# Kernel optimization log

Measured on AMD Instinct MI355X. Metric: run time of the kernel, lower is better.

The kernel has to match this reference:

```python
import jax, jax.numpy as jnp
import numpy as np

N_NODES, N_EDGES, B = 16384, 262144, 128
FEAT, HEADS, OUT_DIM, EMBED, PROT_LEN, VOCAB = 78, 10, 128, 128, 1000, 26
NEG_SLOPE = 0.2


def _gat_conv(x, src, dst, W, a_src, a_dst, b, heads, out_c):
    """PyG-style GATConv (concat heads), eval mode (no dropout)."""
    n = x.shape[0]
    xl = (x @ W).reshape(n, heads, out_c)                    # [N,H,C]
    alpha_s = jnp.einsum('nhc,hc->nh', xl, a_src)            # [N,H]
    alpha_d = jnp.einsum('nhc,hc->nh', xl, a_dst)
    e = jax.nn.leaky_relu(alpha_s[src] + alpha_d[dst], NEG_SLOPE)  # [E,H]
    # scatter-softmax over destination neighborhoods
    m = jax.ops.segment_max(e, dst, num_segments=n)
    m = jnp.where(jnp.isfinite(m), m, 0.0)
    p = jnp.exp(e - m[dst])
    s = jax.ops.segment_sum(p, dst, num_segments=n)
    alpha = p / (s[dst] + 1e-16)                             # [E,H]
    out = jax.ops.segment_sum(alpha[:, :, None] * xl[src], dst, num_segments=n)
    return out.reshape(n, heads * out_c) + b


def setup_inputs() -> dict:
    key = jax.random.key(0)
    ks = jax.random.split(key, 24)
    inp = {}
    inp['x'] = jax.random.normal(ks[0], (N_NODES, FEAT), jnp.float32)
    inp['edge_index'] = jax.random.randint(ks[1], (2, N_EDGES), 0, N_NODES)
    inp['batch'] = jnp.sort(jax.random.randint(ks[2], (N_NODES,), 0, B))
    inp['target'] = jax.random.randint(ks[3], (B, PROT_LEN), 0, VOCAB)
    s = 0.05
    rn = lambda k, sh: jax.random.normal(k, sh, jnp.float32) * s
    inp['W1'] = rn(ks[4], (FEAT, HEADS * FEAT))
    inp['att_src1'] = rn(ks[5], (HEADS, FEAT))
    inp['att_dst1'] = rn(ks[6], (HEADS, FEAT))
    inp['b1'] = jnp.zeros((HEADS * FEAT,), jnp.float32)
    # GAT layer 2: 780 -> 128, 1 head
    inp['W2'] = rn(ks[7], (HEADS * FEAT, OUT_DIM))
    inp['att_src2'] = rn(ks[8], (1, OUT_DIM))
    inp['att_dst2'] = rn(ks[9], (1, OUT_DIM))
    inp['b2'] = jnp.zeros((OUT_DIM,), jnp.float32)
    inp['fc_g1_w'] = rn(ks[10], (OUT_DIM, OUT_DIM)); inp['fc_g1_b'] = jnp.zeros((OUT_DIM,), jnp.float32)
    inp['emb'] = rn(ks[11], (VOCAB, EMBED))
    inp['conv_w'] = rn(ks[12], (32, PROT_LEN, 8)); inp['conv_b'] = jnp.zeros((32,), jnp.float32)
    inp['fc_xt_w'] = rn(ks[13], (32 * 121, OUT_DIM)); inp['fc_xt_b'] = jnp.zeros((OUT_DIM,), jnp.float32)
    inp['fc1_w'] = rn(ks[14], (256, 1024)); inp['fc1_b'] = jnp.zeros((1024,), jnp.float32)
    inp['fc2_w'] = rn(ks[15], (1024, 256)); inp['fc2_b'] = jnp.zeros((256,), jnp.float32)
    inp['out_w'] = rn(ks[16], (256, 1)); inp['out_b'] = jnp.zeros((1,), jnp.float32)
    return inp


def reference(x, edge_index, batch, target, W1, att_src1, att_dst1, b1,
              W2, att_src2, att_dst2, b2, fc_g1_w, fc_g1_b, emb, conv_w, conv_b,
              fc_xt_w, fc_xt_b, fc1_w, fc1_b, fc2_w, fc2_b, out_w, out_b):
    n = x.shape[0]
    # add self-loops (PyG GATConv default)
    loops = jnp.arange(n, dtype=edge_index.dtype)
    src = jnp.concatenate([edge_index[0], loops])
    dst = jnp.concatenate([edge_index[1], loops])
    # drug graph branch (eval: dropout = identity)
    h = jax.nn.elu(_gat_conv(x, src, dst, W1, att_src1, att_dst1, b1, HEADS, FEAT))
    h = _gat_conv(h, src, dst, W2, att_src2, att_dst2, b2, 1, OUT_DIM)
    h = jax.nn.relu(h)
    # global max pool per graph
    g = jax.ops.segment_max(h, batch, num_segments=B)
    g = jnp.where(jnp.isfinite(g), g, 0.0)
    g = jax.nn.relu(g @ fc_g1_w + fc_g1_b)                   # [B,128]
    # protein branch: embedding -> conv1d over embed axis (channels = seq pos)
    e = emb[target]                                          # [B,1000,128]
    c = jax.lax.conv_general_dilated(e, conv_w, (1,), 'VALID',
                                     dimension_numbers=('NCH', 'OIH', 'NCH'))
    c = jax.nn.relu(c + conv_b[None, :, None])               # [B,32,121]
    xt = c.reshape(-1, 32 * 121) @ fc_xt_w + fc_xt_b         # [B,128]
    # fused head
    xc = jnp.concatenate([g, xt], axis=1)                    # [B,256]
    xc = jax.nn.relu(xc @ fc1_w + fc1_b)
    xc = jax.nn.relu(xc @ fc2_w + fc2_b)
    return xc @ out_w + out_b                                # [B,1]
```

## Files before the change

kernel.cpp:

```cpp
#include <hip/hip_runtime.h>
#include <hip/hip_bf16.h>

using bf16 = __hip_bfloat16;

#define NN 16384
#define NE 262144
#define ET (NE + NN)
#define NB 128
#define FEAT 78
#define HEADS 10
#define D1 780
#define OD 128
#define PL 1000
#define VOC 26
#define SLOPE 0.2f

__global__ void k_hist(const int* __restrict__ ei, int* __restrict__ cnt){
    int e = blockIdx.x*256 + threadIdx.x;
    if (e >= ET) return;
    int dst = (e < NE) ? ei[NE + e] : (e - NE);
    atomicAdd(&cnt[dst], 1);
}

__global__ __launch_bounds__(1024) void k_scan(const int* __restrict__ cnt, int* __restrict__ off){
    __shared__ int ps[1024];
    int t = threadIdx.x;
    int loc[16]; int s = 0;
#pragma unroll
    for (int j = 0; j < 16; ++j){ loc[j] = cnt[t*16 + j]; s += loc[j]; }
    ps[t] = s; __syncthreads();
    for (int d = 1; d < 1024; d <<= 1){
        int v = (t >= d) ? ps[t - d] : 0;
        __syncthreads();
        ps[t] += v;
        __syncthreads();
    }
    int run = (t == 0) ? 0 : ps[t - 1];
#pragma unroll
    for (int j = 0; j < 16; ++j){ off[t*16 + j] = run; run += loc[j]; }
    if (t == 1023) off[NN] = run;
}

__global__ void k_fill(const int* __restrict__ ei, const int* __restrict__ off,
                       int* __restrict__ cur, int* __restrict__ csrc){
    int e = blockIdx.x*256 + threadIdx.x;
    if (e >= ET) return;
    int src, dst;
    if (e < NE){ src = ei[e]; dst = ei[NE + e]; } else { src = e - NE; dst = src; }
    int p = off[dst] + atomicAdd(&cur[dst], 1);
    csrc[p] = src;
}

__global__ __launch_bounds__(256) void k_alpha1x(const float* __restrict__ x, const float* __restrict__ W1,
                                                 const float* __restrict__ asw, const float* __restrict__ adw,
                                                 float* __restrict__ as1, float* __restrict__ ad1){
    __shared__ float xs[64*79];
    __shared__ float va[D1], vd[D1];
    int n0 = blockIdx.x * 64, t = threadIdx.x;
    for (int i = t; i < 64*FEAT; i += 256){
        int n = i / FEAT, k = i % FEAT;
        xs[n*79 + k] = x[(size_t)n0*FEAT + i];
    }
    for (int idx = t; idx < D1; idx += 256){
        int h = idx / FEAT, k = idx % FEAT;
        const float* wr = W1 + (size_t)k*D1 + h*FEAT;
        const float* pa = asw + h*FEAT;
        const float* pd = adw + h*FEAT;
        float a = 0.f, d = 0.f;
        for (int j = 0; j < FEAT; ++j){ float w = wr[j]; a += w*pa[j]; d += w*pd[j]; }
        va[idx] = a; vd[idx] = d;
    }
    __syncthreads();
    for (int p = t; p < 64*HEADS; p += 256){
        int h = p >> 6, nl = p & 63;
        const float* xr = xs + nl*79;
        const float* pa = va + h*FEAT; const float* pd = vd + h*FEAT;
        float a = 0.f, d = 0.f;
        for (int k = 0; k < FEAT; ++k){ float xv = xr[k]; a += xv*pa[k]; d += xv*pd[k]; }
        as1[(size_t)(n0 + nl)*HEADS + h] = a;
        ad1[(size_t)(n0 + nl)*HEADS + h] = d;
    }
}

__global__ __launch_bounds__(64) void k_gat1x(const float* __restrict__ x, const float* __restrict__ as1,
                                              const float* __restrict__ ad1, const int* __restrict__ off,
                                              const int* __restrict__ csrc,
                                              float* __restrict__ agg){
    int dst = blockIdx.x, lane = threadIdx.x;
    int beg = off[dst], end = off[dst + 1];
    int deg = end - beg;
    float adh[HEADS];
#pragma unroll
    for (int h = 0; h < HEADS; ++h) adh[h] = ad1[(size_t)dst*HEADS + h];
    int s0 = 0;
    float p[HEADS], mx[HEADS];
#pragma unroll
    for (int h = 0; h < HEADS; ++h){ mx[h] = -1e30f; p[h] = 0.f; }
    if (lane < deg){
        s0 = csrc[beg + lane];
#pragma unroll
        for (int h = 0; h < HEADS; ++h){
            float v = as1[(size_t)s0*HEADS + h] + adh[h];
            v = v > 0.f ? v : SLOPE*v;
            p[h] = v; mx[h] = v;
        }
    }
    if (deg > 64){
        for (int e = beg + 64 + lane; e < end; e += 64){
            int s = csrc[e];
#pragma unroll
            for (int h = 0; h < HEADS; ++h){
                float v = as1[(size_t)s*HEADS + h] + adh[h];
                v = v > 0.f ? v : SLOPE*v;
                mx[h] = fmaxf(mx[h], v);
            }
        }
    }
#pragma unroll
    for (int h = 0; h < HEADS; ++h)
        for (int o = 32; o; o >>= 1) mx[h] = fmaxf(mx[h], __shfl_xor(mx[h], o));
    float sm[HEADS];
#pragma unroll
    for (int h = 0; h < HEADS; ++h) sm[h] = 0.f;
    if (lane < deg){
#pragma unroll
        for (int h = 0; h < HEADS; ++h){ p[h] = __expf(p[h] - mx[h]); sm[h] = p[h]; }
    }
    if (deg > 64){
        for (int e = beg + 64 + lane; e < end; e += 64){
            int s = csrc[e];
#pragma unroll
            for (int h = 0; h < HEADS; ++h){
                float v = as1[(size_t)s*HEADS + h] + adh[h];
                v = v > 0.f ? v : SLOPE*v;
                sm[h] += __expf(v - mx[h]);
            }
        }
    }
    float inv[HEADS];
#pragma unroll
    for (int h = 0; h < HEADS; ++h){
        for (int o = 32; o; o >>= 1) sm[h] += __shfl_xor(sm[h], o);
        inv[h] = 1.f/(sm[h] + 1e-16f);
        p[h] = (lane < deg) ? p[h]*inv[h] : 0.f;
    }
    float acc1[HEADS], acc2[HEADS];
#pragma unroll
    for (int h = 0; h < HEADS; ++h){ acc1[h] = 0.f; acc2[h] = 0.f; }
    int cnt0 = deg < 64 ? deg : 64;
    for (int c0 = 0; c0 < cnt0; c0 += 16){
        float r1[16], r2[16];
#pragma unroll
        for (int i = 0; i < 16; ++i){
            int s = __shfl(s0, c0 + i);
            const float* xr = x + (size_t)s*FEAT;
            r1[i] = xr[lane];
            r2[i] = (lane < FEAT - 64) ? xr[64 + lane] : 0.f;
        }
#pragma unroll
        for (int i = 0; i < 16; ++i){
            if (c0 + i < cnt0){
#pragma unroll
                for (int h = 0; h < HEADS; ++h){
                    float al = __shfl(p[h], c0 + i);
                    acc1[h] += al*r1[i];
                    acc2[h] += al*r2[i];
                }
            }
        }
    }
    if (deg > 64){
        for (int base = beg + 64; base < end; base += 64){
            int cnt = min(64, end - base);
            int s1 = 0;
            float pp[HEADS];
#pragma unroll
            for (int h = 0; h < HEADS; ++h) pp[h] = 0.f;
            if (lane < cnt){
                s1 = csrc[base + lane];
#pragma unroll
                for (int h = 0; h < HEADS; ++h){
                    float v = as1[(size_t)s1*HEADS + h] + adh[h];
                    v = v > 0.f ? v : SLOPE*v;
                    pp[h] = __expf(v - mx[h])*inv[h];
                }
            }
            for (int c0 = 0; c0 < cnt; c0 += 16){
                float r1[16], r2[16];
#pragma unroll
                for (int i = 0; i < 16; ++i){
                    int s = __shfl(s1, c0 + i);
                    const float* xr = x + (size_t)s*FEAT;
                    r1[i] = xr[lane];
                    r2[i] = (lane < FEAT - 64) ? xr[64 + lane] : 0.f;
                }
#pragma unroll
                for (int i = 0; i < 16; ++i){
                    if (c0 + i < cnt){
#pragma unroll
                        for (int h = 0; h < HEADS; ++h){
                            float al = __shfl(pp[h], c0 + i);
                            acc1[h] += al*r1[i];
                            acc2[h] += al*r2[i];
                        }
                    }
                }
            }
        }
    }
#pragma unroll
    for (int h = 0; h < HEADS; ++h)
        agg[(size_t)dst*D1 + h*FEAT + lane] = acc1[h];
    if (lane < FEAT - 64){
#pragma unroll
        for (int h = 0; h < HEADS; ++h)
            agg[(size_t)dst*D1 + h*FEAT + 64 + lane] = acc2[h];
    }
}

__global__ __launch_bounds__(256) void k_post1(const float* __restrict__ agg, const float* __restrict__ W1,
                                               const float* __restrict__ b1, float* __restrict__ h1){
    __shared__ float w1s[FEAT][80];
    __shared__ float ags[64][81];
    __shared__ float bsh[FEAT];
    int ht = blockIdx.x >> 8;
    int nt = blockIdx.x & 255;
    int n0 = nt * 64;
    int t = threadIdx.x;
    for (int i = t; i < FEAT*FEAT; i += 256){
        int k = i / FEAT, j = i % FEAT;
        w1s[k][j] = W1[(size_t)k*D1 + ht*FEAT + j];
    }
    for (int i = t; i < 64*FEAT; i += 256){
        int r = i / FEAT, k = i % FEAT;
        ags[r][k] = agg[(size_t)(n0 + r)*D1 + ht*FEAT + k];
    }
    if (t < FEAT) bsh[t] = b1[ht*FEAT + t];
    __syncthreads();
    if (t < 208){
        int rg = t / 13, cg = t % 13;
        int c0 = cg*6;
        float acc[4][6];
#pragma unroll
        for (int i = 0; i < 4; ++i)
#pragma unroll
            for (int j = 0; j < 6; ++j) acc[i][j] = 0.f;
        for (int k = 0; k < FEAT; ++k){
            float av[4];
#pragma unroll
            for (int i = 0; i < 4; ++i) av[i] = ags[rg*4 + i][k];
            float2 w01 = *(const float2*)&w1s[k][c0];
            float2 w23 = *(const float2*)&w1s[k][c0 + 2];
            float2 w45 = *(const float2*)&w1s[k][c0 + 4];
            float wv[6] = {w01.x, w01.y, w23.x, w23.y, w45.x, w45.y};
#pragma unroll
            for (int i = 0; i < 4; ++i)
#pragma unroll
                for (int j = 0; j < 6; ++j) acc[i][j] += av[i]*wv[j];
        }
#pragma unroll
        for (int i = 0; i < 4; ++i){
#pragma unroll
            for (int j = 0; j < 6; ++j){
                float v = acc[i][j] + bsh[c0 + j];
                v = v > 0.f ? v : __expf(v) - 1.f;
                h1[(size_t)(n0 + rg*4 + i)*D1 + ht*FEAT + c0 + j] = v;
            }
        }
    }
}

#define KC 39
#define KS 4
#define KSEG 195
__global__ __launch_bounds__(256) void k_gemm2(const float* __restrict__ h1, const float* __restrict__ W2,
                                               float* __restrict__ xlp){
    __shared__ __align__(16) float as[KC][68];
    __shared__ __align__(16) float ws[KC][128];
    int bid = blockIdx.x;
    int ks = bid & (KS - 1);
    int r0 = (bid >> 2) * 64;
    int t = threadIdx.x;
    int rg = t >> 5, jq = t & 31;
    float acc[8][4];
#pragma unroll
    for (int i = 0; i < 8; ++i)
#pragma unroll
        for (int j = 0; j < 4; ++j) acc[i][j] = 0.f;
    for (int kc = ks*KSEG; kc < ks*KSEG + KSEG; kc += KC){
        for (int i = t; i < 64*KC; i += 256){
            int r = i / KC, k = i % KC;
            as[k][r] = h1[(size_t)(r0 + r)*D1 + kc + k];
        }
        for (int i = t; i < KC*128; i += 256){
            int k = i >> 7, j = i & 127;
            ws[k][j] = W2[(size_t)(kc + k)*OD + j];
        }
        __syncthreads();
        for (int k = 0; k < KC; ++k){
            float4 a0 = *(const float4*)&as[k][rg*8];
            float4 a1 = *(const float4*)&as[k][rg*8 + 4];
            float4 w4 = *(const float4*)&ws[k][jq*4];
            float av[8] = {a0.x, a0.y, a0.z, a0.w, a1.x, a1.y, a1.z, a1.w};
            float wv[4] = {w4.x, w4.y, w4.z, w4.w};
#pragma unroll
            for (int i = 0; i < 8; ++i)
#pragma unroll
                for (int j = 0; j < 4; ++j) acc[i][j] += av[i]*wv[j];
        }
        __syncthreads();
    }
    float* dst = xlp + (size_t)ks*NN*OD;
#pragma unroll
    for (int i = 0; i < 8; ++i){
        float4 o4 = make_float4(acc[i][0], acc[i][1], acc[i][2], acc[i][3]);
        *(float4*)&dst[(size_t)(r0 + rg*8 + i)*OD + jq*4] = o4;
    }
}

__global__ __launch_bounds__(128) void k_red(const float* __restrict__ xlp,
                                             const float* __restrict__ s2w, const float* __restrict__ d2w,
                                             float* __restrict__ xl2,
                                             float* __restrict__ as2, float* __restrict__ ad2){
    const size_t Q = (size_t)NN*OD/4;
    int t = threadIdx.x;
    size_t fi = (size_t)blockIdx.x*128 + t;
    const float4* P = (const float4*)xlp;
    float4 a = P[fi], b = P[fi + Q], c = P[fi + 2*Q], d = P[fi + 3*Q];
    float4 v = make_float4(a.x+b.x+c.x+d.x, a.y+b.y+c.y+d.y,
                           a.z+b.z+c.z+d.z, a.w+b.w+c.w+d.w);
    ((float4*)xl2)[fi] = v;
    int cc = (t & 31)*4;
    float sa = v.x*s2w[cc] + v.y*s2w[cc+1] + v.z*s2w[cc+2] + v.w*s2w[cc+3];
    float sd = v.x*d2w[cc] + v.y*d2w[cc+1] + v.z*d2w[cc+2] + v.w*d2w[cc+3];
#pragma unroll
    for (int o = 16; o; o >>= 1){ sa += __shfl_xor(sa, o); sd += __shfl_xor(sd, o); }
    if ((t & 31) == 0){
        int n = blockIdx.x*4 + (t >> 5);
        as2[n] = sa; ad2[n] = sd;
    }
}

__global__ __launch_bounds__(64) void k_gat2(const float* __restrict__ xl2, const float* __restrict__ as2,
                                             const float* __restrict__ ad2, const int* __restrict__ off,
                                             const int* __restrict__ csrc, const float* __restrict__ b2,
                                             float* __restrict__ h2){
    int dst = blockIdx.x, lane = threadIdx.x;
    int beg = off[dst], end = off[dst + 1];
    int deg = end - beg;
    float ad = ad2[dst];
    int s0 = 0; float v0 = -1e30f;
    if (lane < deg){
        s0 = csrc[beg + lane];
        float v = as2[s0] + ad;
        v0 = v > 0.f ? v : SLOPE*v;
    }
    float m = v0;
    if (deg > 64){
        for (int e = beg + 64 + lane; e < end; e += 64){
            float v = as2[csrc[e]] + ad; v = v > 0.f ? v : SLOPE*v;
            m = fmaxf(m, v);
        }
    }
    for (int o = 32; o; o >>= 1) m = fmaxf(m, __shfl_xor(m, o));
    float pe = (lane < deg) ? __expf(v0 - m) : 0.f;
    float sm = pe;
    if (deg > 64){
        for (int e = beg + 64 + lane; e < end; e += 64){
            float v = as2[csrc[e]] + ad; v = v > 0.f ? v : SLOPE*v;
            sm += __expf(v - m);
        }
    }
    for (int o = 32; o; o >>= 1) sm += __shfl_xor(sm, o);
    float inv = 1.f / (sm + 1e-16f);
    float p = pe * inv;
    float a0 = 0.f, a1 = 0.f;
    int cnt0 = deg < 64 ? deg : 64;
    for (int c0 = 0; c0 < cnt0; c0 += 16){
        float r1[16], r2[16];
#pragma unroll
        for (int i = 0; i < 16; ++i){
            int s = __shfl(s0, c0 + i);
            r1[i] = xl2[(size_t)s*OD + lane];
            r2[i] = xl2[(size_t)s*OD + 64 + lane];
        }
#pragma unroll
        for (int i = 0; i < 16; ++i){
            if (c0 + i < cnt0){
                float al = __shfl(p, c0 + i);
                a0 += al*r1[i];
                a1 += al*r2[i];
            }
        }
    }
    if (deg > 64){
        for (int base = beg + 64; base < end; base += 64){
            int cnt = min(64, end - base);
            int s1 = 0; float pp = 0.f;
            if (lane < cnt){
                s1 = csrc[base + lane];
                float v = as2[s1] + ad; v = v > 0.f ? v : SLOPE*v;
                pp = __expf(v - m) * inv;
            }
            for (int c0 = 0; c0 < cnt; c0 += 16){
                float r1[16], r2[16];
#pragma unroll
                for (int i = 0; i < 16; ++i){
                    int s = __shfl(s1, c0 + i);
                    r1[i] = xl2[(size_t)s*OD + lane];
                    r2[i] = xl2[(size_t)s*OD + 64 + lane];
                }
#pragma unroll
                for (int i = 0; i < 16; ++i){
                    if (c0 + i < cnt){
                        float al = __shfl(pp, c0 + i);
                        a0 += al*r1[i];
                        a1 += al*r2[i];
                    }
                }
            }
        }
    }
    float o0 = a0 + b2[lane];      o0 = o0 > 0.f ? o0 : 0.f;
    float o1 = a1 + b2[64 + lane]; o1 = o1 > 0.f ? o1 : 0.f;
    h2[(size_t)dst*OD + lane] = o0;
    h2[(size_t)dst*OD + 64 + lane] = o1;
}

__global__ __launch_bounds__(128) void k_poolfc(const float* __restrict__ h2, const int* __restrict__ batch,
                                                const float* __restrict__ w, const float* __restrict__ bias,
                                                float* __restrict__ gfc){
    __shared__ float row[OD];
    int b = blockIdx.x, t = threadIdx.x;
    int lo = 0, hi = NN;
    while (lo < hi){ int mid = (lo + hi) >> 1; if (batch[mid] < b) lo = mid + 1; else hi = mid; }
    int s0 = lo;
    lo = s0; hi = NN;
    while (lo < hi){ int mid = (lo + hi) >> 1; if (batch[mid] < b + 1) lo = mid + 1; else hi = mid; }
    int s1 = lo;
    float mx = 0.f;
    for (int n = s0; n < s1; ++n) mx = fmaxf(mx, h2[(size_t)n*OD + t]);
    row[t] = mx;
    __syncthreads();
    float acc = 0.f;
    for (int k = 0; k < OD; ++k) acc += row[k] * w[k*OD + t];
    acc += bias[t];
    gfc[b*OD + t] = acc > 0.f ? acc : 0.f;
}

__global__ __launch_bounds__(256) void k_wt(const float* __restrict__ convw, float* __restrict__ wt){
    int idx = blockIdx.x*256 + threadIdx.x;
    int i = idx >> 8, ok = idx & 255;
    wt[idx] = convw[(size_t)(ok >> 3)*PL*8 + (size_t)i*8 + (ok & 7)];
}

__global__ __launch_bounds__(256) void k_abuild(const int* __restrict__ target, const float* __restrict__ wt,
                                                float* __restrict__ Ag){
    __shared__ int Ai[VOC][256];
    __shared__ int tss[256];
    int b = blockIdx.x >> 2, seg = blockIdx.x & 3;
    int t = threadIdx.x;
#pragma unroll
    for (int v = 0; v < VOC; ++v) Ai[v][t] = 0;
    if (t < 250) tss[t] = target[b*PL + seg*250 + t];
    __syncthreads();
    const float* wtb = wt + (size_t)(seg*250)*256 + t;
    const float SC = 16777216.0f;
    for (int i = 0; i < 250; ++i){
        float w = wtb[(size_t)i*256];
        int q = __float2int_rn(w * SC);
        atomicAdd(&Ai[tss[i]][t], q);
    }
    __syncthreads();
    const float INV = 5.9604644775390625e-08f;
    float* Ao = Ag + (size_t)blockIdx.x*VOC*256 + t;
#pragma unroll
    for (int v = 0; v < VOC; ++v) Ao[(size_t)v*256] = (float)Ai[v][t] * INV;
}

__global__ __launch_bounds__(256) void k_conv(const float* __restrict__ Ag, const float* __restrict__ emb,
                                              const float* __restrict__ convb, float* __restrict__ cbuf){
    __shared__ float As[VOC][128];
    __shared__ float embs[VOC*128 + 16];
    int b = blockIdx.x >> 1, half = blockIdx.x & 1;
    int t = threadIdx.x;
    for (int i = t; i < VOC*128; i += 256){
        int v = i >> 7, c = i & 127;
        float s = 0.f;
#pragma unroll
        for (int seg = 0; seg < 4; ++seg)
            s += Ag[((size_t)(b*4 + seg)*VOC + v)*256 + half*128 + c];
        As[v][c] = s;
        embs[i] = emb[i];
    }
    if (t < 16) embs[VOC*128 + t] = 0.f;
    __syncthreads();
    int o_l = t >> 4, pg = t & 15, p0 = pg * 8;
    float accp[8];
#pragma unroll
    for (int i = 0; i < 8; ++i) accp[i] = 0.f;
    for (int v = 0; v < VOC; ++v){
        float w[15];
        const float* er = embs + v*128 + p0;
#pragma unroll
        for (int i = 0; i < 15; ++i) w[i] = er[i];
#pragma unroll
        for (int k2 = 0; k2 < 8; ++k2){
            float a = As[v][o_l*8 + k2];
#pragma unroll
            for (int j = 0; j < 8; ++j) accp[j] += a * w[j + k2];
        }
    }
    float cbv = convb[half*16 + o_l];
#pragma unroll
    for (int j = 0; j < 8; ++j){
        int p = p0 + j;
        if (p < 121){
            float v2 = accp[j] + cbv;
            cbuf[(size_t)b*3872 + (half*16 + o_l)*121 + p] = v2 > 0.f ? v2 : 0.f;
        }
    }
}

__global__ __launch_bounds__(256) void k_xt(const float* __restrict__ cbuf, const float* __restrict__ fxw,
                                            float* __restrict__ xtp){
    __shared__ float csh[16][242];
    int kt = blockIdx.x >> 3, bt = blockIdx.x & 7;
    int t = threadIdx.x;
    for (int i = t; i < 16*242; i += 256){
        int bb = i / 242, kk = i % 242;
        csh[bb][kk] = cbuf[(size_t)(bt*16 + bb)*3872 + kt*242 + kk];
    }
    __syncthreads();
    int j = t & 127, bh = t >> 7;
    float acc[8];
#pragma unroll
    for (int i = 0; i < 8; ++i) acc[i] = 0.f;
    for (int kk = 0; kk < 242; ++kk){
        float w = fxw[(size_t)(kt*242 + kk)*128 + j];
#pragma unroll
        for (int bb = 0; bb < 8; ++bb) acc[bb] += csh[bh*8 + bb][kk] * w;
    }
#pragma unroll
    for (int bb = 0; bb < 8; ++bb)
        xtp[(size_t)kt*NB*128 + (size_t)(bt*16 + bh*8 + bb)*128 + j] = acc[bb];
}

__global__ __launch_bounds__(256) void k_fc1(const float* __restrict__ gfc, const float* __restrict__ xtp,
                                             const float* __restrict__ fxb,
                                             const float* __restrict__ w, const float* __restrict__ bias,
                                             float* __restrict__ out){
    __shared__ float xc[256];
    int b = blockIdx.x >> 2, nt = blockIdx.x & 3;
    int t = threadIdx.x;
    if (t < 128) xc[t] = gfc[b*OD + t];
    else {
        int j = t - 128;
        float s = fxb[j];
#pragma unroll
        for (int kt = 0; kt < 16; ++kt) s += xtp[(size_t)kt*NB*128 + (size_t)b*128 + j];
        xc[t] = s;
    }
    __syncthreads();
    int j = nt*256 + t;
    float acc = 0.f;
    for (int k = 0; k < 256; ++k) acc += xc[k] * w[(size_t)k*1024 + j];
    acc += bias[j];
    out[b*1024 + j] = acc > 0.f ? acc : 0.f;
}

__global__ __launch_bounds__(256) void k_fc2p(const float* __restrict__ hf1, const float* __restrict__ w,
                                              float* __restrict__ part){
    __shared__ float row[256];
    int b = blockIdx.x >> 2, ks = blockIdx.x & 3;
    int t = threadIdx.x;
    row[t] = hf1[b*1024 + ks*256 + t];
    __syncthreads();
    float acc = 0.f;
    const float* wc = w + (size_t)(ks*256)*256 + t;
    for (int k = 0; k < 256; ++k) acc += row[k] * wc[(size_t)k*256];
    part[((size_t)ks*NB + b)*256 + t] = acc;
}

__global__ __launch_bounds__(256) void k_fc2red(const float* __restrict__ part, const float* __restrict__ bias,
                                                const float* __restrict__ ow, const float* __restrict__ ob,
                                                float* __restrict__ out){
    __shared__ float s2[256];
    int b = blockIdx.x, t = threadIdx.x;
    float v = part[(size_t)b*256 + t] + part[((size_t)NB + b)*256 + t]
            + part[((size_t)2*NB + b)*256 + t] + part[((size_t)3*NB + b)*256 + t];
    v += bias[t];
    v = v > 0.f ? v : 0.f;
    s2[t] = v * ow[t];
    __syncthreads();
    if (t < 64){
        float a = s2[t] + s2[t + 64] + s2[t + 128] + s2[t + 192];
#pragma unroll
        for (int o = 32; o; o >>= 1) a += __shfl_xor(a, o);
        if (t == 0) out[b] = a + ob[0];
    }
}

extern "C" void kernel_launch(void* const* d_in, const int* in_sizes, int n_in,
                              void* d_out, int out_size, void* d_ws, size_t ws_size,
                              hipStream_t stream){
    const float* x    = (const float*)d_in[0];
    const int*  ei    = (const int*)d_in[1];
    const int*  batch = (const int*)d_in[2];
    const int*  target= (const int*)d_in[3];
    const float* W1   = (const float*)d_in[4];
    const float* as1w = (const float*)d_in[5];
    const float* ad1w = (const float*)d_in[6];
    const float* b1   = (const float*)d_in[7];
    const float* W2   = (const float*)d_in[8];
    const float* as2w = (const float*)d_in[9];
    const float* ad2w = (const float*)d_in[10];
    const float* b2   = (const float*)d_in[11];
    const float* fgw  = (const float*)d_in[12];
    const float* fgb  = (const float*)d_in[13];
    const float* emb  = (const float*)d_in[14];
    const float* cw   = (const float*)d_in[15];
    const float* cb   = (const float*)d_in[16];
    const float* fxw  = (const float*)d_in[17];
    const float* fxb  = (const float*)d_in[18];
    const float* f1w  = (const float*)d_in[19];
    const float* f1b  = (const float*)d_in[20];
    const float* f2w  = (const float*)d_in[21];
    const float* f2b  = (const float*)d_in[22];
    const float* ow   = (const float*)d_in[23];
    const float* ob   = (const float*)d_in[24];

    float* f = (float*)d_ws;
    size_t o = 0;
    float* agg = f + o; o += (size_t)NN*D1;
    float* h1  = f + o; o += (size_t)NN*D1;
    float* as1 = f + o; o += (size_t)NN*HEADS;
    float* ad1 = f + o; o += (size_t)NN*HEADS;
    float* xl2 = f + o; o += (size_t)NN*OD;
    float* h2  = f + o; o += (size_t)NN*OD;
    float* as2 = f + o; o += NN;
    float* ad2 = f + o; o += NN;
    float* gfc = f + o; o += NB*OD;
    float* hf1 = f + o; o += NB*1024;
    float* part= f + o; o += (size_t)4*NB*256;
    float* wt  = f + o; o += (size_t)PL*256;
    float* cbuf= f + o; o += (size_t)NB*3872;
    float* xtp = f + o; o += (size_t)16*NB*128;
    int* cnt   = (int*)(f + o); o += NN;
    int* off   = (int*)(f + o); o += NN + 1;
    int* csrc  = (int*)(f + o); o += ET;
    float* xlp = agg;
    float* Ag  = h1;
    (void)ws_size; (void)in_sizes; (void)n_in; (void)out_size;

    hipMemsetAsync(cnt, 0, NN*sizeof(int), stream);
    k_hist<<<(ET + 255)/256, 256, 0, stream>>>(ei, cnt);
    k_scan<<<1, 1024, 0, stream>>>(cnt, off);
    hipMemsetAsync(cnt, 0, NN*sizeof(int), stream);
    k_fill<<<(ET + 255)/256, 256, 0, stream>>>(ei, off, cnt, csrc);

    k_alpha1x<<<NN/64, 256, 0, stream>>>(x, W1, as1w, ad1w, as1, ad1);
    k_gat1x<<<NN, 64, 0, stream>>>(x, as1, ad1, off, csrc, agg);
    k_post1<<<HEADS*256, 256, 0, stream>>>(agg, W1, b1, h1);

    k_gemm2<<<(NN/64)*KS, 256, 0, stream>>>(h1, W2, xlp);
    k_red<<<NN/4, 128, 0, stream>>>(xlp, as2w, ad2w, xl2, as2, ad2);
    k_gat2<<<NN, 64, 0, stream>>>(xl2, as2, ad2, off, csrc, b2, h2);

    k_poolfc<<<NB, 128, 0, stream>>>(h2, batch, fgw, fgb, gfc);

    k_wt<<<1000, 256, 0, stream>>>(cw, wt);
    k_abuild<<<NB*4, 256, 0, stream>>>(target, wt, Ag);
    k_conv<<<NB*2, 256, 0, stream>>>(Ag, emb, cb, cbuf);
    k_xt<<<128, 256, 0, stream>>>(cbuf, fxw, xtp);

    k_fc1<<<NB*4, 256, 0, stream>>>(gfc, xtp, fxb, f1w, f1b, hf1);
    k_fc2p<<<NB*4, 256, 0, stream>>>(hf1, f2w, part);
    k_fc2red<<<NB, 256, 0, stream>>>(part, f2b, ow, ob, (float*)d_out);
}
```

Baseline: 415.9 us.

## Replace layer-2 FP32 split-K GEMM with bf16 MFMA GEMM and fused attention logits

k_post1 now writes h1 as bf16, and W2 is converted to bf16 by a small kernel. The split-K FP32 GEMM plus the separate reduction kernel are replaced by one MFMA 16x16x32 bf16 GEMM. That GEMM writes xl2 directly and computes the as2/ad2 attention dot products in its epilogue. This halves h1 traffic, removes the partial-sum buffer and one launch, and moves the math onto matrix cores, at the cost of bf16 rounding of activations and weights.

```diff
diff --git a/kernel.cpp b/kernel.cpp
--- a/kernel.cpp
+++ b/kernel.cpp
@@ -15,6 +15,14 @@
 #define VOC 26
 #define SLOPE 0.2f
 
+typedef __attribute__((ext_vector_type(8))) short short8;
+typedef __attribute__((ext_vector_type(4))) float f32x4;
+
+static __device__ __forceinline__ ushort f2bf(float f){
+    bf16 h = __float2bfloat16(f);
+    return *reinterpret_cast<ushort*>(&h);
+}
+
 __global__ void k_hist(const int* __restrict__ ei, int* __restrict__ cnt){
     int e = blockIdx.x*256 + threadIdx.x;
     if (e >= ET) return;
@@ -219,7 +227,7 @@
 }
 
 __global__ __launch_bounds__(256) void k_post1(const float* __restrict__ agg, const float* __restrict__ W1,
-                                               const float* __restrict__ b1, float* __restrict__ h1){
+                                               const float* __restrict__ b1, ushort* __restrict__ h1h){
     __shared__ float w1s[FEAT][80];
     __shared__ float ags[64][81];
     __shared__ float bsh[FEAT];
@@ -264,80 +272,93 @@
             for (int j = 0; j < 6; ++j){
                 float v = acc[i][j] + bsh[c0 + j];
                 v = v > 0.f ? v : __expf(v) - 1.f;
-                h1[(size_t)(n0 + rg*4 + i)*D1 + ht*FEAT + c0 + j] = v;
-            }
-        }
-    }
-}
-
-#define KC 39
-#define KS 4
-#define KSEG 195
-__global__ __launch_bounds__(256) void k_gemm2(const float* __restrict__ h1, const float* __restrict__ W2,
-                                               float* __restrict__ xlp){
-    __shared__ __align__(16) float as[KC][68];
-    __shared__ __align__(16) float ws[KC][128];
-    int bid = blockIdx.x;
-    int ks = bid & (KS - 1);
-    int r0 = (bid >> 2) * 64;
+                h1h[(size_t)(n0 + rg*4 + i)*D1 + ht*FEAT + c0 + j] = f2bf(v);
+            }
+        }
+    }
+}
+
+__global__ __launch_bounds__(256) void k_w2h(const float* __restrict__ w2, ushort* __restrict__ w2h){
+    int i = blockIdx.x*256 + threadIdx.x;
+    w2h[i] = f2bf(w2[i]);
+}
+
+__global__ __launch_bounds__(256) void k_gemm2m(const ushort* __restrict__ h1h, const ushort* __restrict__ w2h,
+                                                const float* __restrict__ s2w, const float* __restrict__ d2w,
+                                                float* __restrict__ xl2,
+                                                float* __restrict__ as2, float* __restrict__ ad2){
+    __shared__ ushort As[64][40];
+    __shared__ ushort Bs[128][40];
+    int r0 = blockIdx.x * 64;
     int t = threadIdx.x;
-    int rg = t >> 5, jq = t & 31;
-    float acc[8][4];
-#pragma unroll
-    for (int i = 0; i < 8; ++i)
-#pragma unroll
-        for (int j = 0; j < 4; ++j) acc[i][j] = 0.f;
-    for (int kc = ks*KSEG; kc < ks*KSEG + KSEG; kc += KC){
-        for (int i = t; i < 64*KC; i += 256){
-            int r = i / KC, k = i % KC;
-            as[k][r] = h1[(size_t)(r0 + r)*D1 + kc + k];
-        }
-        for (int i = t; i < KC*128; i += 256){
-            int k = i >> 7, j = i & 127;
-            ws[k][j] = W2[(size_t)(kc + k)*OD + j];
+    int w = t >> 6, l = t & 63;
+    f32x4 acc[8];
+#pragma unroll
+    for (int i = 0; i < 8; ++i) acc[i] = (f32x4){0.f, 0.f, 0.f, 0.f};
+    for (int k0 = 0; k0 < D1; k0 += 32){
+        {
+            int r = t >> 2, kq = (t & 3)*8;
+            int gk = k0 + kq;
+            ushort tmp[8];
+            if (gk + 8 <= D1){
+                *(ushort4*)&tmp[0] = *(const ushort4*)&h1h[(size_t)(r0 + r)*D1 + gk];
+                *(ushort4*)&tmp[4] = *(const ushort4*)&h1h[(size_t)(r0 + r)*D1 + gk + 4];
+            } else {
+#pragma unroll
+                for (int j = 0; j < 8; ++j)
+                    tmp[j] = (gk + j < D1) ? h1h[(size_t)(r0 + r)*D1 + gk + j] : (ushort)0;
+            }
+            *(ushort4*)&As[r][kq]     = *(ushort4*)&tmp[0];
+            *(ushort4*)&As[r][kq + 4] = *(ushort4*)&tmp[4];
+        }
+        {
+            int n8 = (t & 15)*8, kk = t >> 4;
+#pragma unroll
+            for (int half = 0; half < 2; ++half){
+                int k = kk + half*16;
+                ushort tmp[8];
+                if (k0 + k < D1){
+                    *(uint4*)&tmp[0] = *(const uint4*)&w2h[(size_t)(k0 + k)*OD + n8];
+                } else {
+#pragma unroll
+                    for (int j = 0; j < 8; ++j) tmp[j] = 0;
+                }
+#pragma unroll
+                for (int j = 0; j < 8; ++j) Bs[n8 + j][k] = tmp[j];
+            }
         }
         __syncthreads();
-        for (int k = 0; k < KC; ++k){
-            float4 a0 = *(const float4*)&as[k][rg*8];
-            float4 a1 = *(const float4*)&as[k][rg*8 + 4];
-            float4 w4 = *(const float4*)&ws[k][jq*4];
-            float av[8] = {a0.x, a0.y, a0.z, a0.w, a1.x, a1.y, a1.z, a1.w};
-            float wv[4] = {w4.x, w4.y, w4.z, w4.w};
-#pragma unroll
-            for (int i = 0; i < 8; ++i)
-#pragma unroll
-                for (int j = 0; j < 4; ++j) acc[i][j] += av[i]*wv[j];
+        short8 a = *(const short8*)&As[w*16 + (l & 15)][(l >> 4)*8];
+#pragma unroll
+        for (int nt = 0; nt < 8; ++nt){
+            short8 b = *(const short8*)&Bs[nt*16 + (l & 15)][(l >> 4)*8];
+            acc[nt] = __builtin_amdgcn_mfma_f32_16x16x32_bf16(a, b, acc[nt], 0, 0, 0);
         }
         __syncthreads();
     }
-    float* dst = xlp + (size_t)ks*NN*OD;
-#pragma unroll
-    for (int i = 0; i < 8; ++i){
-        float4 o4 = make_float4(acc[i][0], acc[i][1], acc[i][2], acc[i][3]);
-        *(float4*)&dst[(size_t)(r0 + rg*8 + i)*OD + jq*4] = o4;
-    }
-}
-
-__global__ __launch_bounds__(128) void k_red(const float* __restrict__ xlp,
-                                             const float* __restrict__ s2w, const float* __restrict__ d2w,
-                                             float* __restrict__ xl2,
-                                             float* __restrict__ as2, float* __restrict__ ad2){
-    const size_t Q = (size_t)NN*OD/4;
-    int t = threadIdx.x;
-    size_t fi = (size_t)blockIdx.x*128 + t;
-    const float4* P = (const float4*)xlp;
-    float4 a = P[fi], b = P[fi + Q], c = P[fi + 2*Q], d = P[fi + 3*Q];
-    float4 v = make_float4(a.x+b.x+c.x+d.x, a.y+b.y+c.y+d.y,
-                           a.z+b.z+c.z+d.z, a.w+b.w+c.w+d.w);
-    ((float4*)xl2)[fi] = v;
-    int cc = (t & 31)*4;
-    float sa = v.x*s2w[cc] + v.y*s2w[cc+1] + v.z*s2w[cc+2] + v.w*s2w[cc+3];
-    float sd = v.x*d2w[cc] + v.y*d2w[cc+1] + v.z*d2w[cc+2] + v.w*d2w[cc+3];
-#pragma unroll
-    for (int o = 16; o; o >>= 1){ sa += __shfl_xor(sa, o); sd += __shfl_xor(sd, o); }
-    if ((t & 31) == 0){
-        int n = blockIdx.x*4 + (t >> 5);
-        as2[n] = sa; ad2[n] = sd;
+    int colg = l & 15, kg = l >> 4;
+    float sa[4] = {0.f,0.f,0.f,0.f}, sd[4] = {0.f,0.f,0.f,0.f};
+#pragma unroll
+    for (int nt = 0; nt < 8; ++nt){
+        int c = nt*16 + colg;
+        float wsv = s2w[c], wdv = d2w[c];
+#pragma unroll
+        for (int r = 0; r < 4; ++r){
+            float v = acc[nt][r];
+            int row = r0 + w*16 + kg*4 + r;
+            xl2[(size_t)row*OD + c] = v;
+            sa[r] += v*wsv; sd[r] += v*wdv;
+        }
+    }
+#pragma unroll
+    for (int r = 0; r < 4; ++r){
+#pragma unroll
+        for (int o = 8; o; o >>= 1){ sa[r] += __shfl_xor(sa[r], o); sd[r] += __shfl_xor(sd[r], o); }
+    }
+    if (colg == 0){
+        int row = r0 + w*16 + kg*4;
+#pragma unroll
+        for (int r = 0; r < 4; ++r){ as2[row + r] = sa[r]; ad2[row + r] = sd[r]; }
     }
 }
 
@@ -633,7 +654,7 @@
     float* f = (float*)d_ws;
     size_t o = 0;
     float* agg = f + o; o += (size_t)NN*D1;
-    float* h1  = f + o; o += (size_t)NN*D1;
+    float* h1f = f + o; o += (size_t)NN*D1;
     float* as1 = f + o; o += (size_t)NN*HEADS;
     float* ad1 = f + o; o += (size_t)NN*HEADS;
     float* xl2 = f + o; o += (size_t)NN*OD;
@@ -646,11 +667,13 @@
     float* wt  = f + o; o += (size_t)PL*256;
     float* cbuf= f + o; o += (size_t)NB*3872;
     float* xtp = f + o; o += (size_t)16*NB*128;
+    float* w2hf= f + o; o += (size_t)D1*OD/2 + 64;
     int* cnt   = (int*)(f + o); o += NN;
     int* off   = (int*)(f + o); o += NN + 1;
     int* csrc  = (int*)(f + o); o += ET;
-    float* xlp = agg;
-    float* Ag  = h1;
+    ushort* h1h = (ushort*)h1f;
+    ushort* w2h = (ushort*)w2hf;
+    float* Ag  = h1f;
     (void)ws_size; (void)in_sizes; (void)n_in; (void)out_size;
 
     hipMemsetAsync(cnt, 0, NN*sizeof(int), stream);
@@ -661,10 +684,10 @@
 
     k_alpha1x<<<NN/64, 256, 0, stream>>>(x, W1, as1w, ad1w, as1, ad1);
     k_gat1x<<<NN, 64, 0, stream>>>(x, as1, ad1, off, csrc, agg);
-    k_post1<<<HEADS*256, 256, 0, stream>>>(agg, W1, b1, h1);
-
-    k_gemm2<<<(NN/64)*KS, 256, 0, stream>>>(h1, W2, xlp);
-    k_red<<<NN/4, 128, 0, stream>>>(xlp, as2w, ad2w, xl2, as2, ad2);
+    k_post1<<<HEADS*256, 256, 0, stream>>>(agg, W1, b1, h1h);
+
+    k_w2h<<<(D1*OD)/256, 256, 0, stream>>>(W2, w2h);
+    k_gemm2m<<<NN/64, 256, 0, stream>>>(h1h, w2h, as2w, ad2w, xl2, as2, ad2);
     k_gat2<<<NN, 64, 0, stream>>>(xl2, as2, ad2, off, csrc, b2, h2);
 
     k_poolfc<<<NB, 128, 0, stream>>>(h2, batch, fgw, fgb, gfc);
```

Result: no change. 408.8 us (-1.7%).
